# Kernel tuning notes

Hardware: AMD Instinct MI355X
Metric: run time of the kernel (lower is better)

Reference implementation:

```python
import jax, jax.numpy as jnp
import numpy as np

N, D, H = 16384, 16, 128  # N samples, d dimensions, mlp hidden


def setup_inputs() -> dict:
    key = jax.random.key(0)
    ks = jax.random.split(key, 4)
    inputs = jax.random.uniform(ks[0], (N, 1 + 2 * D), dtype=jnp.float32)  # col 0 = step size h > 0
    W1 = jax.random.normal(ks[1], (D, H), dtype=jnp.float32) * 0.1
    b1 = jnp.zeros((H,), jnp.float32)
    Wm = jax.random.normal(ks[2], (H, D), dtype=jnp.float32) * 0.1
    bm = jnp.zeros((D,), jnp.float32)
    Ws = jax.random.normal(ks[3], (H, D), dtype=jnp.float32) * 0.1
    bs = jnp.zeros((D,), jnp.float32)
    return {"inputs": inputs, "W1": W1, "b1": b1, "Wm": Wm, "bm": bm, "Ws": Ws, "bs": bs}


def _test_normality(samples):
    # BHEP statistic Tn. samples: [N, d].
    n = samples.shape[0]
    d = samples.shape[1]
    Rj2 = jnp.sum(samples * samples, axis=-1)                    # [N]
    # ||s_j - s_k||^2 via norm expansion (avoids N x N x d intermediate)
    Rjk = Rj2[:, None] + Rj2[None, :] - 2.0 * (samples @ samples.T)  # [N, N]
    Rjk = jnp.maximum(Rjk, 0.0)
    Tn0 = jnp.sum(jnp.exp(-0.5 * Rjk)) / n
    Tn1 = -(2.0 ** (1.0 - d / 2.0)) * jnp.sum(jnp.exp(-0.25 * Rj2))
    Tn2 = n * (3.0 ** (-d / 2.0))
    return Tn0 + Tn1 + Tn2


def reference(inputs, W1, b1, Wm, bm, Ws, bs):
    d = (inputs.shape[1] - 1) // 2
    step = inputs[:, :1]                # [N, 1] step size h
    x_n = inputs[:, 1:1 + d]            # [N, d]
    x_np1 = inputs[:, 1 + d:]           # [N, d]
    # inner model: mean / positive scale heads
    h = jax.nn.relu(x_n @ W1 + b1)
    approx_mean = h @ Wm + bm
    approx_scale = jax.nn.softplus(h @ Ws + bs) + 1e-3
    # euler_maruyama_sampler
    batch_samples = (x_np1 - (x_n + step * approx_mean)) / (jnp.sqrt(step) * approx_scale)
    return _test_normality(batch_samples)
```

## Files before the change

### kernel.cpp

```cpp
#include <hip/hip_runtime.h>
#include <math.h>

#define NROWS 16384
#define DD 16
#define HH 128
#define NSUP 64
#define NPAIRS 2080
#define L2E 1.4426950408889634f
#define SQL2E 1.2011224087864498f

typedef __attribute__((ext_vector_type(8))) short v8s;
typedef __attribute__((ext_vector_type(4))) float v4f;
typedef __attribute__((ext_vector_type(4))) unsigned int v4u;

__device__ __forceinline__ float softplus_f(float x) {
    return fmaxf(x, 0.0f) + log1pf(__expf(-fabsf(x)));
}
__device__ __forceinline__ float exp2_b(float x) {
#if __has_builtin(__builtin_amdgcn_exp2f)
    return __builtin_amdgcn_exp2f(x);
#else
    return exp2f(x);
#endif
}
__device__ __forceinline__ unsigned short bf16_rne(float f) {
    unsigned int u = __float_as_uint(f);
    return (unsigned short)((u + 0x7FFFu + ((u >> 16) & 1u)) >> 16);
}

__global__ __launch_bounds__(512) void prep_kernel(
    const float* __restrict__ inputs,
    const float* __restrict__ W1, const float* __restrict__ b1,
    const float* __restrict__ Wm, const float* __restrict__ bm,
    const float* __restrict__ Ws, const float* __restrict__ bs,
    unsigned int* __restrict__ packed,
    float* __restrict__ hvals,
    float* __restrict__ tpart)
{
    __shared__ v4f sW1t4[HH * 4];
    __shared__ v4f sWm4[HH * 4], sWs4[HH * 4];
    __shared__ float sb1[HH];
    __shared__ float part[DD][512];
    int tid = threadIdx.x;

    {
        const v4f* gm = (const v4f*)Wm;
        const v4f* gs = (const v4f*)Ws;
        for (int i = tid; i < HH * 4; i += 512) { sWm4[i] = gm[i]; sWs4[i] = gs[i]; }
        float* sW1t = (float*)sW1t4;
        for (int i = tid; i < DD * HH; i += 512) {
            int d = i >> 7, u = i & 127;
            sW1t[u * DD + d] = W1[i];
        }
        if (tid < HH) sb1[tid] = b1[tid];
    }
    __syncthreads();

    int t = tid & 63, w = tid >> 6;
    int row = blockIdx.x * 64 + t;
    const float* rp = inputs + row * (1 + 2 * DD);
    float x[DD];
    #pragma unroll
    for (int d = 0; d < DD; ++d) x[d] = rp[1 + d];
    v4f m4[4], s4[4];
    #pragma unroll
    for (int q = 0; q < 4; ++q)
        #pragma unroll
        for (int r = 0; r < 4; ++r) { m4[q][r] = 0.0f; s4[q][r] = 0.0f; }

    int u0 = w * 16;
    for (int u = u0; u < u0 + 16; ++u) {
        v4f a0 = sW1t4[u * 4 + 0], a1 = sW1t4[u * 4 + 1];
        v4f a2 = sW1t4[u * 4 + 2], a3 = sW1t4[u * 4 + 3];
        float hv = sb1[u];
        #pragma unroll
        for (int r = 0; r < 4; ++r) hv = fmaf(x[r], a0[r], hv);
        #pragma unroll
        for (int r = 0; r < 4; ++r) hv = fmaf(x[4 + r], a1[r], hv);
        #pragma unroll
        for (int r = 0; r < 4; ++r) hv = fmaf(x[8 + r], a2[r], hv);
        #pragma unroll
        for (int r = 0; r < 4; ++r) hv = fmaf(x[12 + r], a3[r], hv);
        hv = fmaxf(hv, 0.0f);
        #pragma unroll
        for (int q = 0; q < 4; ++q) {
            v4f wm = sWm4[u * 4 + q], ws = sWs4[u * 4 + q];
            #pragma unroll
            for (int r = 0; r < 4; ++r) {
                m4[q][r] = fmaf(hv, wm[r], m4[q][r]);
                s4[q][r] = fmaf(hv, ws[r], s4[q][r]);
            }
        }
    }

    #pragma unroll
    for (int d = 0; d < DD; ++d) part[d][tid] = m4[d >> 2][d & 3];
    __syncthreads();
    float mm[DD];
    if (w == 0) {
        #pragma unroll
        for (int d = 0; d < DD; ++d) {
            mm[d] = ((part[d][t] + part[d][64 + t]) + (part[d][128 + t] + part[d][192 + t]))
                  + ((part[d][256 + t] + part[d][320 + t]) + (part[d][384 + t] + part[d][448 + t]))
                  + bm[d];
        }
    }
    __syncthreads();
    #pragma unroll
    for (int d = 0; d < DD; ++d) part[d][tid] = s4[d >> 2][d & 3];
    __syncthreads();

    if (w == 0) {
        float step = rp[0];
        float ss = sqrtf(step);
        float r2 = 0.0f;
        float smp[DD];
        #pragma unroll
        for (int d = 0; d < DD; ++d) {
            float sv = ((part[d][t] + part[d][64 + t]) + (part[d][128 + t] + part[d][192 + t]))
                     + ((part[d][256 + t] + part[d][320 + t]) + (part[d][384 + t] + part[d][448 + t]))
                     + bs[d];
            float sp = softplus_f(sv) + 0.001f;
            smp[d] = (rp[1 + DD + d] - (x[d] + step * mm[d])) / (ss * sp);
            r2 = fmaf(smp[d], smp[d], r2);
        }
        hvals[row] = -0.5f * r2 * L2E;

        float t1 = __expf(-0.25f * r2);
        #pragma unroll
        for (int off = 32; off > 0; off >>= 1) t1 += __shfl_down(t1, off);
        if (t == 0) tpart[blockIdx.x] = t1;

        unsigned short hs[DD], ls[DD];
        #pragma unroll
        for (int d = 0; d < DD; ++d) {
            float sp2 = smp[d] * SQL2E;
            unsigned short hi = bf16_rne(sp2);
            float rem = sp2 - __uint_as_float(((unsigned int)hi) << 16);
            hs[d] = hi;
            ls[d] = bf16_rne(rem);
        }
        unsigned int* prow = packed + row * 16;
        v4u q;
        q.x = hs[0] | (hs[1] << 16);  q.y = hs[2] | (hs[3] << 16);
        q.z = hs[4] | (hs[5] << 16);  q.w = hs[6] | (hs[7] << 16);
        *(v4u*)(prow + 0) = q;
        q.x = hs[8] | (hs[9] << 16);  q.y = hs[10] | (hs[11] << 16);
        q.z = hs[12] | (hs[13] << 16); q.w = hs[14] | (hs[15] << 16);
        *(v4u*)(prow + 4) = q;
        q.x = ls[0] | (ls[1] << 16);  q.y = ls[2] | (ls[3] << 16);
        q.z = ls[4] | (ls[5] << 16);  q.w = ls[6] | (ls[7] << 16);
        *(v4u*)(prow + 8) = q;
        q.x = ls[8] | (ls[9] << 16);  q.y = ls[10] | (ls[11] << 16);
        q.z = ls[12] | (ls[13] << 16); q.w = ls[14] | (ls[15] << 16);
        *(v4u*)(prow + 12) = q;
    }
}

__global__ __launch_bounds__(256, 2) void pair_kernel(
    const unsigned int* __restrict__ packed,
    const float* __restrict__ hvals,
    float* __restrict__ ppart)
{
    __shared__ unsigned short skB[8192];
    __shared__ float shk[256];
    __shared__ float shj[256];
    __shared__ float red[4];

    int tid = threadIdx.x;
    int l = tid & 63, w = tid >> 6;

    int p = blockIdx.x;
    int a = 0;
    while (p >= NSUP - a) { p -= NSUP - a; ++a; }
    int b = a + p;
    bool isdiag = (a == b);

    int jbase = a * 256 + w * 64;
    int kb = b * 256;

    int col = l & 15;
    int sub = l >> 4;
    int myrow4 = sub * 4;

    const unsigned short* pk16 = (const unsigned short*)packed;

    shj[tid] = hvals[a * 256 + tid];
    shk[tid] = hvals[kb + tid];
    #pragma unroll
    for (int c = 0; c < 4; ++c) {
        int chunk = c * 256 + tid;
        int tt = chunk >> 6, l6 = chunk & 63;
        int rec = kb + tt * 16 + (l6 & 15);
        int sk = l6 >> 4;
        v8s v = *(const v8s*)(pk16 + (size_t)rec * 32 + sk * 8);
        *(v8s*)(skB + chunk * 8) = v;
    }

    v8s A1[4], A2[4];
    #pragma unroll
    for (int f = 0; f < 4; ++f) {
        int jrow = jbase + f * 16 + col;
        A1[f] = *(const v8s*)(pk16 + (size_t)jrow * 32 + sub * 8);
        A2[f] = *(const v8s*)(pk16 + (size_t)jrow * 32 + (sub ^ 2) * 8);
    }
    __syncthreads();

    v4f hj4[4];
    #pragma unroll
    for (int f = 0; f < 4; ++f)
        hj4[f] = *(const v4f*)&shj[w * 64 + f * 16 + myrow4];

    float sum0 = 0.0f, sum1 = 0.0f, sum2 = 0.0f, sum3 = 0.0f;
    const v8s* skB8 = (const v8s*)skB;

    #pragma unroll 2
    for (int tt = 0; tt < 16; tt += 2) {
        v8s Ba = skB8[tt * 64 + l];
        v8s Bb = skB8[(tt + 1) * 64 + l];
        float hka = shk[tt * 16 + col];
        float hkb = shk[(tt + 1) * 16 + col];

        #pragma unroll
        for (int fp = 0; fp < 2; ++fp) {
            const int f0 = 2 * fp, f1 = 2 * fp + 1;
            v4f c0a, c1a, c0b, c1b;
            #pragma unroll
            for (int r = 0; r < 4; ++r) {
                c0a[r] = hj4[f0][r] + hka; c1a[r] = hj4[f1][r] + hka;
                c0b[r] = hj4[f0][r] + hkb; c1b[r] = hj4[f1][r] + hkb;
            }
            c0a = __builtin_amdgcn_mfma_f32_16x16x32_bf16(A1[f0], Ba, c0a, 0, 0, 0);
            c1a = __builtin_amdgcn_mfma_f32_16x16x32_bf16(A1[f1], Ba, c1a, 0, 0, 0);
            c0b = __builtin_amdgcn_mfma_f32_16x16x32_bf16(A1[f0], Bb, c0b, 0, 0, 0);
            c1b = __builtin_amdgcn_mfma_f32_16x16x32_bf16(A1[f1], Bb, c1b, 0, 0, 0);
            c0a = __builtin_amdgcn_mfma_f32_16x16x32_bf16(A2[f0], Ba, c0a, 0, 0, 0);
            c1a = __builtin_amdgcn_mfma_f32_16x16x32_bf16(A2[f1], Ba, c1a, 0, 0, 0);
            c0b = __builtin_amdgcn_mfma_f32_16x16x32_bf16(A2[f0], Bb, c0b, 0, 0, 0);
            c1b = __builtin_amdgcn_mfma_f32_16x16x32_bf16(A2[f1], Bb, c1b, 0, 0, 0);

            float e0 = exp2_b(c0a[0]), e1 = exp2_b(c0a[1]);
            float e2 = exp2_b(c0a[2]), e3 = exp2_b(c0a[3]);
            float e4 = exp2_b(c1a[0]), e5 = exp2_b(c1a[1]);
            float e6 = exp2_b(c1a[2]), e7 = exp2_b(c1a[3]);
            float g0 = exp2_b(c0b[0]), g1 = exp2_b(c0b[1]);
            float g2 = exp2_b(c0b[2]), g3 = exp2_b(c0b[3]);
            float g4 = exp2_b(c1b[0]), g5 = exp2_b(c1b[1]);
            float g6 = exp2_b(c1b[2]), g7 = exp2_b(c1b[3]);

            if (isdiag) {
                if (tt == w * 4 + f0) {
                    if (myrow4 + 0 == col) e0 = 0.0f;
                    if (myrow4 + 1 == col) e1 = 0.0f;
                    if (myrow4 + 2 == col) e2 = 0.0f;
                    if (myrow4 + 3 == col) e3 = 0.0f;
                }
                if (tt == w * 4 + f1) {
                    if (myrow4 + 0 == col) e4 = 0.0f;
                    if (myrow4 + 1 == col) e5 = 0.0f;
                    if (myrow4 + 2 == col) e6 = 0.0f;
                    if (myrow4 + 3 == col) e7 = 0.0f;
                }
                if (tt + 1 == w * 4 + f0) {
                    if (myrow4 + 0 == col) g0 = 0.0f;
                    if (myrow4 + 1 == col) g1 = 0.0f;
                    if (myrow4 + 2 == col) g2 = 0.0f;
                    if (myrow4 + 3 == col) g3 = 0.0f;
                }
                if (tt + 1 == w * 4 + f1) {
                    if (myrow4 + 0 == col) g4 = 0.0f;
                    if (myrow4 + 1 == col) g5 = 0.0f;
                    if (myrow4 + 2 == col) g6 = 0.0f;
                    if (myrow4 + 3 == col) g7 = 0.0f;
                }
            }
            float esA0 = (e0 + e1) + (e2 + e3);
            float esA1 = (e4 + e5) + (e6 + e7);
            float esB0 = (g0 + g1) + (g2 + g3);
            float esB1 = (g4 + g5) + (g6 + g7);
            if (fp == 0) { sum0 += esA0 + esB0; sum1 += esA1 + esB1; }
            else         { sum2 += esA0 + esB0; sum3 += esA1 + esB1; }
        }
    }

    float v = (sum0 + sum1) + (sum2 + sum3);
    #pragma unroll
    for (int off = 32; off > 0; off >>= 1) v += __shfl_down(v, off);
    if (l == 0) red[w] = v;
    __syncthreads();
    if (tid == 0) {
        float wgt = isdiag ? 1.0f : 2.0f;
        ppart[blockIdx.x] = wgt * (red[0] + red[1] + red[2] + red[3]);
    }
}

__global__ __launch_bounds__(256) void final_kernel(
    const float* __restrict__ ppart, const float* __restrict__ tpart,
    float* __restrict__ out)
{
    __shared__ float reds[4], redt[4];
    int tid = threadIdx.x;
    int l = tid & 63, w = tid >> 6;

    float s = 0.0f;
    for (int i = tid; i < NPAIRS; i += 256) s += ppart[i];
    float t = tpart[tid];

    #pragma unroll
    for (int off = 32; off > 0; off >>= 1) {
        s += __shfl_down(s, off);
        t += __shfl_down(t, off);
    }
    if (l == 0) { reds[w] = s; redt[w] = t; }
    __syncthreads();
    if (tid == 0) {
        float S = (reds[0] + reds[1]) + (reds[2] + reds[3]);
        float T = (redt[0] + redt[1]) + (redt[2] + redt[3]);
        float n = (float)NROWS;
        out[0] = (S + n) / n - 0.0078125f * T + n * (1.0f / 6561.0f);
    }
}

extern "C" void kernel_launch(void* const* d_in, const int* in_sizes, int n_in,
                              void* d_out, int out_size, void* d_ws, size_t ws_size,
                              hipStream_t stream)
{
    const float* inputs = (const float*)d_in[0];
    const float* W1 = (const float*)d_in[1];
    const float* b1 = (const float*)d_in[2];
    const float* Wm = (const float*)d_in[3];
    const float* bm = (const float*)d_in[4];
    const float* Ws = (const float*)d_in[5];
    const float* bs = (const float*)d_in[6];

    float* tpart         = (float*)((char*)d_ws + 256);
    float* ppart         = (float*)((char*)d_ws + 256 + 1024);
    float* hvals         = (float*)((char*)d_ws + 256 + 1024 + 8448);
    unsigned int* packed = (unsigned int*)((char*)d_ws + 256 + 1024 + 8448 + 65536);

    prep_kernel<<<NROWS / 64, 512, 0, stream>>>(inputs, W1, b1, Wm, bm, Ws, bs,
                                                packed, hvals, tpart);
    pair_kernel<<<NPAIRS, 256, 0, stream>>>(packed, hvals, ppart);
    final_kernel<<<1, 256, 0, stream>>>(ppart, tpart, (float*)d_out);
}
```

Before: 45.60 us.

## Process two tile pairs per block with register prefetch of the next K tile

After: 49.37 us. 1.08x slower.

```diff
diff --git a/kernel.cpp b/kernel.cpp
--- a/kernel.cpp
+++ b/kernel.cpp
@@ -157,62 +157,11 @@
     }
 }
 
-__global__ __launch_bounds__(256, 2) void pair_kernel(
-    const unsigned int* __restrict__ packed,
-    const float* __restrict__ hvals,
-    float* __restrict__ ppart)
-{
-    __shared__ unsigned short skB[8192];
-    __shared__ float shk[256];
-    __shared__ float shj[256];
-    __shared__ float red[4];
-
-    int tid = threadIdx.x;
-    int l = tid & 63, w = tid >> 6;
-
-    int p = blockIdx.x;
-    int a = 0;
-    while (p >= NSUP - a) { p -= NSUP - a; ++a; }
-    int b = a + p;
-    bool isdiag = (a == b);
-
-    int jbase = a * 256 + w * 64;
-    int kb = b * 256;
-
-    int col = l & 15;
-    int sub = l >> 4;
-    int myrow4 = sub * 4;
-
-    const unsigned short* pk16 = (const unsigned short*)packed;
-
-    shj[tid] = hvals[a * 256 + tid];
-    shk[tid] = hvals[kb + tid];
-    #pragma unroll
-    for (int c = 0; c < 4; ++c) {
-        int chunk = c * 256 + tid;
-        int tt = chunk >> 6, l6 = chunk & 63;
-        int rec = kb + tt * 16 + (l6 & 15);
-        int sk = l6 >> 4;
-        v8s v = *(const v8s*)(pk16 + (size_t)rec * 32 + sk * 8);
-        *(v8s*)(skB + chunk * 8) = v;
-    }
-
-    v8s A1[4], A2[4];
-    #pragma unroll
-    for (int f = 0; f < 4; ++f) {
-        int jrow = jbase + f * 16 + col;
-        A1[f] = *(const v8s*)(pk16 + (size_t)jrow * 32 + sub * 8);
-        A2[f] = *(const v8s*)(pk16 + (size_t)jrow * 32 + (sub ^ 2) * 8);
-    }
-    __syncthreads();
-
-    v4f hj4[4];
-    #pragma unroll
-    for (int f = 0; f < 4; ++f)
-        hj4[f] = *(const v4f*)&shj[w * 64 + f * 16 + myrow4];
-
+__device__ __forceinline__ float compute16(
+    const v8s* skB8, const float* shk, const v8s* A1, const v8s* A2,
+    const v4f* hj4, bool isdiag, int w, int myrow4, int col, int l)
+{
     float sum0 = 0.0f, sum1 = 0.0f, sum2 = 0.0f, sum3 = 0.0f;
-    const v8s* skB8 = (const v8s*)skB;
 
     #pragma unroll 2
     for (int tt = 0; tt < 16; tt += 2) {
@@ -282,15 +231,118 @@
             else         { sum2 += esA0 + esB0; sum3 += esA1 + esB1; }
         }
     }
-
-    float v = (sum0 + sum1) + (sum2 + sum3);
-    #pragma unroll
-    for (int off = 32; off > 0; off >>= 1) v += __shfl_down(v, off);
-    if (l == 0) red[w] = v;
-    __syncthreads();
-    if (tid == 0) {
-        float wgt = isdiag ? 1.0f : 2.0f;
-        ppart[blockIdx.x] = wgt * (red[0] + red[1] + red[2] + red[3]);
+    return (sum0 + sum1) + (sum2 + sum3);
+}
+
+__global__ __launch_bounds__(256, 2) void pair_kernel(
+    const unsigned int* __restrict__ packed,
+    const float* __restrict__ hvals,
+    float* __restrict__ ppart)
+{
+    __shared__ unsigned short skB[8192];
+    __shared__ float shk[256];
+    __shared__ float shj[256];
+    __shared__ float red[4];
+
+    int tid = threadIdx.x;
+    int l = tid & 63, w = tid >> 6;
+
+    int p = (int)blockIdx.x * 2;
+    int a0 = 0;
+    while (p >= NSUP - a0) { p -= NSUP - a0; ++a0; }
+    int b0 = a0 + p;
+    int a1 = a0, b1 = b0 + 1;
+    if (b1 >= NSUP) { a1 = a0 + 1; b1 = a1; }
+
+    int col = l & 15;
+    int sub = l >> 4;
+    int myrow4 = sub * 4;
+
+    const unsigned short* pk16 = (const unsigned short*)packed;
+
+    shj[tid] = hvals[a0 * 256 + tid];
+    shk[tid] = hvals[b0 * 256 + tid];
+    int kb0 = b0 * 256;
+    #pragma unroll
+    for (int c = 0; c < 4; ++c) {
+        int chunk = c * 256 + tid;
+        int tt = chunk >> 6, l6 = chunk & 63;
+        int rec = kb0 + tt * 16 + (l6 & 15);
+        int sk = l6 >> 4;
+        *(v8s*)(skB + chunk * 8) = *(const v8s*)(pk16 + (size_t)rec * 32 + sk * 8);
+    }
+    v8s A1[4], A2[4];
+    #pragma unroll
+    for (int f = 0; f < 4; ++f) {
+        int jrow = a0 * 256 + w * 64 + f * 16 + col;
+        A1[f] = *(const v8s*)(pk16 + (size_t)jrow * 32 + sub * 8);
+        A2[f] = *(const v8s*)(pk16 + (size_t)jrow * 32 + (sub ^ 2) * 8);
+    }
+    __syncthreads();
+
+    v4f hj4[4];
+    #pragma unroll
+    for (int f = 0; f < 4; ++f)
+        hj4[f] = *(const v4f*)&shj[w * 64 + f * 16 + myrow4];
+
+    v8s pf[4];
+    float pfhk;
+    {
+        int kb1 = b1 * 256;
+        #pragma unroll
+        for (int c = 0; c < 4; ++c) {
+            int chunk = c * 256 + tid;
+            int tt = chunk >> 6, l6 = chunk & 63;
+            int rec = kb1 + tt * 16 + (l6 & 15);
+            int sk = l6 >> 4;
+            pf[c] = *(const v8s*)(pk16 + (size_t)rec * 32 + sk * 8);
+        }
+        pfhk = hvals[kb1 + tid];
+    }
+
+    {
+        float v = compute16((const v8s*)skB, shk, A1, A2, hj4, a0 == b0, w, myrow4, col, l);
+        #pragma unroll
+        for (int off = 32; off > 0; off >>= 1) v += __shfl_down(v, off);
+        if (l == 0) red[w] = v;
+        __syncthreads();
+        if (tid == 0) {
+            float wgt = (a0 == b0) ? 1.0f : 2.0f;
+            ppart[(int)blockIdx.x * 2] = wgt * (red[0] + red[1] + red[2] + red[3]);
+        }
+        __syncthreads();
+    }
+
+    #pragma unroll
+    for (int c = 0; c < 4; ++c)
+        *(v8s*)(skB + (c * 256 + tid) * 8) = pf[c];
+    shk[tid] = pfhk;
+    if (a1 != a0) {
+        shj[tid] = hvals[a1 * 256 + tid];
+        #pragma unroll
+        for (int f = 0; f < 4; ++f) {
+            int jrow = a1 * 256 + w * 64 + f * 16 + col;
+            A1[f] = *(const v8s*)(pk16 + (size_t)jrow * 32 + sub * 8);
+            A2[f] = *(const v8s*)(pk16 + (size_t)jrow * 32 + (sub ^ 2) * 8);
+        }
+    }
+    __syncthreads();
+    if (a1 != a0) {
+        #pragma unroll
+        for (int f = 0; f < 4; ++f)
+            hj4[f] = *(const v4f*)&shj[w * 64 + f * 16 + myrow4];
+    }
+
+    {
+        float v = compute16((const v8s*)skB, shk, A1, A2, hj4, a1 == b1, w, myrow4, col, l);
+        #pragma unroll
+        for (int off = 32; off > 0; off >>= 1) v += __shfl_down(v, off);
+        if (l == 0) red[w] = v;
+        __syncthreads();
+        if (tid == 0) {
+            float wgt = (a1 == b1) ? 1.0f : 2.0f;
+            ppart[(int)blockIdx.x * 2 + 1] = wgt * (red[0] + red[1] + red[2] + red[3]);
+        }
     }
 }
 
@@ -340,6 +392,6 @@
 
     prep_kernel<<<NROWS / 64, 512, 0, stream>>>(inputs, W1, b1, Wm, bm, Ws, bs,
                                                 packed, hvals, tpart);
-    pair_kernel<<<NPAIRS, 256, 0, stream>>>(packed, hvals, ppart);
+    pair_kernel<<<NPAIRS / 2, 256, 0, stream>>>(packed, hvals, ppart);
     final_kernel<<<1, 256, 0, stream>>>(ppart, tpart, (float*)d_out);
 }
```
